# Kernel tuning notes

Hardware: AMD Instinct MI355X
Metric: run time of the kernel (lower is better)

Reference implementation:

```python
import jax, jax.numpy as jnp
import numpy as np

B, T_IN, F_IN, H, T_OUT = 1024, 168, 8, 256, 96


def setup_inputs() -> dict:
    key = jax.random.key(0)
    ks = jax.random.split(key, 12)
    s = 1.0 / np.sqrt(H)  # torch LSTM/Linear default init scale
    return {
        "inputs": jax.random.normal(ks[0], (B, T_IN, F_IN), jnp.float32),
        "enc_Wih": jax.random.normal(ks[1], (4 * H, F_IN), jnp.float32) * s,
        "enc_Whh": jax.random.normal(ks[2], (4 * H, H), jnp.float32) * s,
        "enc_bih": jax.random.normal(ks[3], (4 * H,), jnp.float32) * s,
        "enc_bhh": jax.random.normal(ks[4], (4 * H,), jnp.float32) * s,
        "dec_Wih": jax.random.normal(ks[5], (4 * H, 1), jnp.float32) * s,
        "dec_Whh": jax.random.normal(ks[6], (4 * H, H), jnp.float32) * s,
        "dec_bih": jax.random.normal(ks[7], (4 * H,), jnp.float32) * s,
        "dec_bhh": jax.random.normal(ks[8], (4 * H,), jnp.float32) * s,
        "fc_W": jax.random.normal(ks[9], (1, H), jnp.float32) * s,
        "fc_b": jax.random.normal(ks[10], (1,), jnp.float32) * s,
    }


def _lstm_cell(x, h, c, Wih, Whh, bih, bhh):
    # PyTorch gate order: input, forget, cell(g), output
    gates = x @ Wih.T + h @ Whh.T + (bih + bhh)  # [B, 4H]
    i, f, g, o = jnp.split(gates, 4, axis=-1)
    c_new = jax.nn.sigmoid(f) * c + jax.nn.sigmoid(i) * jnp.tanh(g)
    h_new = jax.nn.sigmoid(o) * jnp.tanh(c_new)
    return h_new, c_new


def reference(inputs, enc_Wih, enc_Whh, enc_bih, enc_bhh,
              dec_Wih, dec_Whh, dec_bih, dec_bhh, fc_W, fc_b):
    batch = inputs.shape[0]
    hidden = inputs.shape[1] and enc_Whh.shape[1]
    h0 = jnp.zeros((batch, enc_Whh.shape[1]), inputs.dtype)
    c0 = jnp.zeros_like(h0)

    # ---- encoder: scan over input time steps ----
    def enc_step(carry, x_t):
        h, c = carry
        h, c = _lstm_cell(x_t, h, c, enc_Wih, enc_Whh, enc_bih, enc_bhh)
        return (h, c), None

    (h, c), _ = jax.lax.scan(enc_step, (h0, c0),
                             jnp.swapaxes(inputs, 0, 1))  # [T,B,F]

    x0 = inputs[:, -1, 0:1]  # [B,1] last value of main feature

    def dec_step(carry, _):
        x, h, c = carry
        h, c = _lstm_cell(x, h, c, dec_Wih, dec_Whh, dec_bih, dec_bhh)
        pred = h @ fc_W.T + fc_b  # [B,1]
        return (pred, h, c), pred

    _, preds = jax.lax.scan(dec_step, (x0, h, c), None, length=T_OUT)
    # preds: [T_OUT, B, 1] -> [B, T_OUT, 1]
    return jnp.swapaxes(preds, 0, 1)
```

## Files before the change

kernel.cpp:

```cpp
#include <hip/hip_runtime.h>


typedef _Float16 f16x8 __attribute__((ext_vector_type(8)));
typedef float f32x4 __attribute__((ext_vector_type(4)));

#define WPW  36864
#define NSTEPS_ENC 168
#define NSTEPS_DEC 96

__device__ __forceinline__ float sigm(float x) {
    float e = __builtin_amdgcn_exp2f(-1.4426950408889634f * x);
    return __builtin_amdgcn_rcpf(1.0f + e);
}
__device__ __forceinline__ float tanh_f(float x) {
    float e = __builtin_amdgcn_exp2f(-2.8853900817779268f * x);
    return 2.0f * __builtin_amdgcn_rcpf(1.0f + e) - 1.0f;
}

__device__ __forceinline__ void mfma8(f32x4 acc[8], f16x8 a, const f16x8 b[8]) {
#pragma unroll
    for (int nt = 0; nt < 8; ++nt)
        acc[nt] = __builtin_amdgcn_mfma_f32_16x16x32_f16(a, b[nt], acc[nt], 0, 0, 0);
}

__device__ __forceinline__ void gemm_all(f32x4 acc[8],
                                         const f16x8 wr[5][8],
                                         const f16x8 (*Bw)[64],
                                         const f16x8 (*K8w)[16],
                                         const _Float16* __restrict__ wp,
                                         const char* ab, int abase,
                                         const _Float16* xsrow,
                                         int lane, int l15, int lg) {
    f16x8 s5[8];
#pragma unroll
    for (int nt = 0; nt < 8; ++nt)
        s5[nt] = *(const f16x8*)(wp + ((5 * 8 + nt) * 64 + lane) * 8);

#pragma unroll
    for (int kt = 0; kt < 5; ++kt) {
        f16x8 a = *(const f16x8*)(ab + abase + kt * 64);
        mfma8(acc, a, wr[kt]);
    }
    {
        f16x8 a = *(const f16x8*)(ab + abase + 5 * 64);
        mfma8(acc, a, s5);
    }
#pragma unroll
    for (int kt = 6; kt < 8; ++kt) {
        f16x8 a = *(const f16x8*)(ab + abase + kt * 64);
#pragma unroll
        for (int nt = 0; nt < 8; ++nt)
            acc[nt] = __builtin_amdgcn_mfma_f32_16x16x32_f16(a, Bw[(kt - 6) * 8 + nt][lane], acc[nt], 0, 0, 0);
    }
    {
        f16x8 a = *(const f16x8*)xsrow;
        _Float16 m = (_Float16)(lg == 0 ? 1.0f : 0.0f);
#pragma unroll
        for (int nt = 0; nt < 8; ++nt) {
            f16x8 b = K8w[nt][l15] * m;
            acc[nt] = __builtin_amdgcn_mfma_f32_16x16x32_f16(a, b, acc[nt], 0, 0, 0);
        }
    }
}


__global__ void k_convert_x(const float* __restrict__ in, _Float16* __restrict__ xf16) {
    int idx = blockIdx.x * 256 + threadIdx.x;
    if (idx >= 168 * 1024 * 8) return;
    int f = idx & 7;
    int b = (idx >> 3) & 1023;
    int t = idx >> 13;
    xf16[idx] = (_Float16)in[(b * 168 + t) * 8 + f];
}

__global__ void k_pack_w(const float* __restrict__ Whh, const float* __restrict__ Wih,
                         int IN, _Float16* __restrict__ Wp) {
    int idx = blockIdx.x * 256 + threadIdx.x;
    if (idx >= 294912) return;
    int j    = idx & 7;
    int lane = (idx >> 3) & 63;
    int nt   = (idx >> 9) & 7;
    int kt   = (idx >> 12) % 9;
    int wv   = idx / 36864;
    int n = (nt >> 1) * 256 + wv * 32 + (nt & 1) * 16 + (lane & 15);
    int k = kt * 32 + (lane >> 4) * 8 + j;
    float v = 0.0f;
    if (k < 256)            v = Whh[n * 256 + k];
    else if (k - 256 < IN)  v = Wih[n * IN + (k - 256)];
    Wp[idx] = (_Float16)v;
}


__global__ __launch_bounds__(512, 2) void lstm_seq2seq(
    const _Float16* __restrict__ xf16,
    const _Float16* __restrict__ WpE,
    const _Float16* __restrict__ WpD,
    const float* __restrict__ bihE, const float* __restrict__ bhhE,
    const float* __restrict__ bihD, const float* __restrict__ bhhD,
    const float* __restrict__ fcW,
    const float* __restrict__ fcb,
    float* __restrict__ out) {

    __shared__ f16x8 Blds[8][16][64];
    __shared__ f16x8 K8[8][8][16];
    __shared__ _Float16 Abuf[16 * 256];
    __shared__ _Float16 xs[16][8];
    __shared__ float partial[8][16];

    const int tid  = threadIdx.x;
    const int lane = tid & 63;
    const int wv   = tid >> 6;
    const int l15  = lane & 15;
    const int lg   = lane >> 4;
    const int b0   = blockIdx.x * 16;

    const char* ab = (const char*)Abuf;
    const int abase = l15 * 512 + ((lg * 16) ^ ((l15 & 3) << 4));

    for (int i = tid; i < 16 * 256; i += 512) Abuf[i] = (_Float16)0.0f;

    const _Float16* wpe = WpE + wv * WPW;
    const _Float16* wpd = WpD + wv * WPW;

    f16x8 wr[5][8];
#pragma unroll
    for (int kt = 0; kt < 5; ++kt)
#pragma unroll
        for (int nt = 0; nt < 8; ++nt)
            wr[kt][nt] = *(const f16x8*)(wpe + ((kt * 8 + nt) * 64 + lane) * 8);
#pragma unroll
    for (int kt = 6; kt < 8; ++kt)
#pragma unroll
        for (int nt = 0; nt < 8; ++nt)
            Blds[wv][(kt - 6) * 8 + nt][lane] = *(const f16x8*)(wpe + ((kt * 8 + nt) * 64 + lane) * 8);
    if (lane < 16) {
#pragma unroll
        for (int nt = 0; nt < 8; ++nt)
            K8[wv][nt][lane] = *(const f16x8*)(wpe + ((8 * 8 + nt) * 64 + lane) * 8);
    }
    float bia[8];
#pragma unroll
    for (int nt = 0; nt < 8; ++nt) {
        int n = (nt >> 1) * 256 + wv * 32 + (nt & 1) * 16 + l15;
        bia[nt] = bihE[n] + bhhE[n];
    }

    float c_st[2][4] = {{0.f,0.f,0.f,0.f},{0.f,0.f,0.f,0.f}};

    __syncthreads();
    if (tid < 128) {
        int m = tid >> 3, f = tid & 7;
        xs[m][f] = xf16[(size_t)(b0 + m) * 8 + f];
    }
    __syncthreads();

#pragma unroll 1
    for (int t = 0; t < NSTEPS_ENC; ++t) {
        f32x4 acc[8];
#pragma unroll
        for (int nt = 0; nt < 8; ++nt) { f32x4 z = {0.f,0.f,0.f,0.f}; acc[nt] = z; }

        _Float16 xh = (_Float16)0.0f;
        if (t < NSTEPS_ENC - 1 && tid < 128)
            xh = xf16[(size_t)((t + 1) * 1024 + b0 + (tid >> 3)) * 8 + (tid & 7)];

        gemm_all(acc, wr, Blds[wv], K8[wv], wpe, ab, abase, &xs[l15][0], lane, l15, lg);

        float hnv[2][4];
#pragma unroll
        for (int half = 0; half < 2; ++half) {
#pragma unroll
            for (int r = 0; r < 4; ++r) {
                float iv = acc[0 + half][r] + bia[0 + half];
                float fv = acc[2 + half][r] + bia[2 + half];
                float gv = acc[4 + half][r] + bia[4 + half];
                float ov = acc[6 + half][r] + bia[6 + half];
                float cn = sigm(fv) * c_st[half][r] + sigm(iv) * tanh_f(gv);
                c_st[half][r] = cn;
                hnv[half][r] = sigm(ov) * tanh_f(cn);
            }
        }
        __syncthreads();
#pragma unroll
        for (int half = 0; half < 2; ++half) {
#pragma unroll
            for (int r = 0; r < 4; ++r) {
                int row = lg * 4 + r;
                int colb = (wv * 32 + half * 16 + l15) * 2;
                *(_Float16*)((char*)Abuf + row * 512 + (colb ^ ((r & 3) << 4))) = (_Float16)hnv[half][r];
            }
        }
        if (t < NSTEPS_ENC - 1) {
            if (tid < 128) xs[tid >> 3][tid & 7] = xh;
        } else {
            if (tid < 16) {
#pragma unroll
                for (int f = 1; f < 8; ++f) xs[tid][f] = (_Float16)0.0f;
            }
        }
        __syncthreads();
    }

#pragma unroll
    for (int kt = 0; kt < 5; ++kt)
#pragma unroll
        for (int nt = 0; nt < 8; ++nt)
            wr[kt][nt] = *(const f16x8*)(wpd + ((kt * 8 + nt) * 64 + lane) * 8);
#pragma unroll
    for (int kt = 6; kt < 8; ++kt)
#pragma unroll
        for (int nt = 0; nt < 8; ++nt)
            Blds[wv][(kt - 6) * 8 + nt][lane] = *(const f16x8*)(wpd + ((kt * 8 + nt) * 64 + lane) * 8);
    if (lane < 16) {
#pragma unroll
        for (int nt = 0; nt < 8; ++nt)
            K8[wv][nt][lane] = *(const f16x8*)(wpd + ((8 * 8 + nt) * 64 + lane) * 8);
    }
#pragma unroll
    for (int nt = 0; nt < 8; ++nt) {
        int n = (nt >> 1) * 256 + wv * 32 + (nt & 1) * 16 + l15;
        bia[nt] = bihD[n] + bhhD[n];
    }
    float fcw0 = fcW[wv * 32 + l15];
    float fcw1 = fcW[wv * 32 + 16 + l15];
    float fcbv = fcb[0];
    __syncthreads();

#pragma unroll 1
    for (int s = 0; s < NSTEPS_DEC; ++s) {
        f32x4 acc[8];
#pragma unroll
        for (int nt = 0; nt < 8; ++nt) { f32x4 z = {0.f,0.f,0.f,0.f}; acc[nt] = z; }

        gemm_all(acc, wr, Blds[wv], K8[wv], wpd, ab, abase, &xs[l15][0], lane, l15, lg);

        float hnv[2][4];
#pragma unroll
        for (int half = 0; half < 2; ++half) {
#pragma unroll
            for (int r = 0; r < 4; ++r) {
                float iv = acc[0 + half][r] + bia[0 + half];
                float fv = acc[2 + half][r] + bia[2 + half];
                float gv = acc[4 + half][r] + bia[4 + half];
                float ov = acc[6 + half][r] + bia[6 + half];
                float cn = sigm(fv) * c_st[half][r] + sigm(iv) * tanh_f(gv);
                c_st[half][r] = cn;
                hnv[half][r] = sigm(ov) * tanh_f(cn);
            }
        }
#pragma unroll
        for (int r = 0; r < 4; ++r) {
            float pv = hnv[0][r] * fcw0 + hnv[1][r] * fcw1;
            pv += __shfl_xor(pv, 1);
            pv += __shfl_xor(pv, 2);
            pv += __shfl_xor(pv, 4);
            pv += __shfl_xor(pv, 8);
            if (l15 == 0) partial[wv][lg * 4 + r] = pv;
        }
        __syncthreads();
#pragma unroll
        for (int half = 0; half < 2; ++half) {
#pragma unroll
            for (int r = 0; r < 4; ++r) {
                int row = lg * 4 + r;
                int colb = (wv * 32 + half * 16 + l15) * 2;
                *(_Float16*)((char*)Abuf + row * 512 + (colb ^ ((r & 3) << 4))) = (_Float16)hnv[half][r];
            }
        }
        if (tid < 16) {
            float pr = fcbv;
#pragma unroll
            for (int w = 0; w < 8; ++w) pr += partial[w][tid];
            out[(size_t)(b0 + tid) * 96 + s] = pr;
            xs[tid][0] = (_Float16)pr;
        }
        __syncthreads();
    }
}


extern "C" void kernel_launch(void* const* d_in, const int* in_sizes, int n_in,
                              void* d_out, int out_size, void* d_ws, size_t ws_size,
                              hipStream_t stream) {
    const float* inputs  = (const float*)d_in[0];
    const float* enc_Wih = (const float*)d_in[1];
    const float* enc_Whh = (const float*)d_in[2];
    const float* enc_bih = (const float*)d_in[3];
    const float* enc_bhh = (const float*)d_in[4];
    const float* dec_Wih = (const float*)d_in[5];
    const float* dec_Whh = (const float*)d_in[6];
    const float* dec_bih = (const float*)d_in[7];
    const float* dec_bhh = (const float*)d_in[8];
    const float* fc_W    = (const float*)d_in[9];
    const float* fc_b    = (const float*)d_in[10];

    char* ws = (char*)d_ws;
    _Float16* xf16 = (_Float16*)(ws);
    _Float16* WpE  = (_Float16*)(ws + 2752512);
    _Float16* WpD  = (_Float16*)(ws + 2752512 + 589824);

    k_convert_x<<<dim3(5376), dim3(256), 0, stream>>>(inputs, xf16);
    k_pack_w<<<dim3(1152), dim3(256), 0, stream>>>(enc_Whh, enc_Wih, 8, WpE);
    k_pack_w<<<dim3(1152), dim3(256), 0, stream>>>(dec_Whh, dec_Wih, 1, WpD);

    lstm_seq2seq<<<dim3(64), dim3(512), 0, stream>>>(
        xf16, WpE, WpD, enc_bih, enc_bhh, dec_bih, dec_bhh, fc_W, fc_b, (float*)d_out);
}
```

Baseline: 1.123 ms.

## Double-buffer hidden state and fuse encoder/decoder loops with one barrier per step

Merges the encoder and decoder loops into one time loop and double-buffers the hidden-state LDS tile, the input tile and the FC partials, so each step needs one __syncthreads instead of two. It folds the bias into the accumulator init and adds the scalar decoder input as an FMA in fp32 rather than an extra MFMA tile. It also redistributes the FC reduction so every wave recomputes the prediction locally, and changes the LDS swizzle to an 8-way XOR. A leftover dead kernel stub with placeholder assignments remains, and the unified loop adds branches on the encoder/decoder flag.

```diff
diff --git a/kernel.cpp b/kernel.cpp
--- a/kernel.cpp
+++ b/kernel.cpp
@@ -5,8 +5,8 @@
 typedef float f32x4 __attribute__((ext_vector_type(4)));
 
 #define WPW  36864
-#define NSTEPS_ENC 168
-#define NSTEPS_DEC 96
+#define NENC 168
+#define NTOT 264
 
 __device__ __forceinline__ float sigm(float x) {
     float e = __builtin_amdgcn_exp2f(-1.4426950408889634f * x);
@@ -16,51 +16,12 @@
     float e = __builtin_amdgcn_exp2f(-2.8853900817779268f * x);
     return 2.0f * __builtin_amdgcn_rcpf(1.0f + e) - 1.0f;
 }
-
+__device__ __forceinline__ f32x4 mfma(f16x8 a, f16x8 b, f32x4 c) {
+    return __builtin_amdgcn_mfma_f32_16x16x32_f16(a, b, c, 0, 0, 0);
+}
 __device__ __forceinline__ void mfma8(f32x4 acc[8], f16x8 a, const f16x8 b[8]) {
 #pragma unroll
-    for (int nt = 0; nt < 8; ++nt)
-        acc[nt] = __builtin_amdgcn_mfma_f32_16x16x32_f16(a, b[nt], acc[nt], 0, 0, 0);
-}
-
-__device__ __forceinline__ void gemm_all(f32x4 acc[8],
-                                         const f16x8 wr[5][8],
-                                         const f16x8 (*Bw)[64],
-                                         const f16x8 (*K8w)[16],
-                                         const _Float16* __restrict__ wp,
-                                         const char* ab, int abase,
-                                         const _Float16* xsrow,
-                                         int lane, int l15, int lg) {
-    f16x8 s5[8];
-#pragma unroll
-    for (int nt = 0; nt < 8; ++nt)
-        s5[nt] = *(const f16x8*)(wp + ((5 * 8 + nt) * 64 + lane) * 8);
-
-#pragma unroll
-    for (int kt = 0; kt < 5; ++kt) {
-        f16x8 a = *(const f16x8*)(ab + abase + kt * 64);
-        mfma8(acc, a, wr[kt]);
-    }
-    {
-        f16x8 a = *(const f16x8*)(ab + abase + 5 * 64);
-        mfma8(acc, a, s5);
-    }
-#pragma unroll
-    for (int kt = 6; kt < 8; ++kt) {
-        f16x8 a = *(const f16x8*)(ab + abase + kt * 64);
-#pragma unroll
-        for (int nt = 0; nt < 8; ++nt)
-            acc[nt] = __builtin_amdgcn_mfma_f32_16x16x32_f16(a, Bw[(kt - 6) * 8 + nt][lane], acc[nt], 0, 0, 0);
-    }
-    {
-        f16x8 a = *(const f16x8*)xsrow;
-        _Float16 m = (_Float16)(lg == 0 ? 1.0f : 0.0f);
-#pragma unroll
-        for (int nt = 0; nt < 8; ++nt) {
-            f16x8 b = K8w[nt][l15] * m;
-            acc[nt] = __builtin_amdgcn_mfma_f32_16x16x32_f16(a, b, acc[nt], 0, 0, 0);
-        }
-    }
+    for (int nt = 0; nt < 8; ++nt) acc[nt] = mfma(a, b[nt], acc[nt]);
 }
 
 
@@ -91,21 +52,20 @@
 }
 
 
-__global__ __launch_bounds__(512, 2) void lstm_seq2seq(
+__global__ __launch_bounds__(512, 2) void lstm6(
+    const float* __restrict__ in0,
     const _Float16* __restrict__ xf16,
     const _Float16* __restrict__ WpE,
     const _Float16* __restrict__ WpD,
     const float* __restrict__ bihE, const float* __restrict__ bhhE,
     const float* __restrict__ bihD, const float* __restrict__ bhhD,
-    const float* __restrict__ fcW,
-    const float* __restrict__ fcb,
+    const float* __restrict__ fcW, const float* __restrict__ fcb,
     float* __restrict__ out) {
 
     __shared__ f16x8 Blds[8][16][64];
-    __shared__ f16x8 K8[8][8][16];
-    __shared__ _Float16 Abuf[16 * 256];
-    __shared__ _Float16 xs[16][8];
-    __shared__ float partial[8][16];
+    __shared__ _Float16 A[2][16 * 256];
+    __shared__ f16x8 xs[2][16];
+    __shared__ f32x4 partial[2][16][2];
 
     const int tid  = threadIdx.x;
     const int lane = tid & 63;
@@ -114,169 +74,214 @@
     const int lg   = lane >> 4;
     const int b0   = blockIdx.x * 16;
 
-    const char* ab = (const char*)Abuf;
-    const int abase = l15 * 512 + ((lg * 16) ^ ((l15 & 3) << 4));
-
-    for (int i = tid; i < 16 * 256; i += 512) Abuf[i] = (_Float16)0.0f;
-
     const _Float16* wpe = WpE + wv * WPW;
     const _Float16* wpd = WpD + wv * WPW;
+    const _Float16* wp8 = wpe + 64 * 512;
 
     f16x8 wr[5][8];
 #pragma unroll
     for (int kt = 0; kt < 5; ++kt)
 #pragma unroll
         for (int nt = 0; nt < 8; ++nt)
-            wr[kt][nt] = *(const f16x8*)(wpe + ((kt * 8 + nt) * 64 + lane) * 8);
+            wr[kt][nt] = *(const f16x8*)(wpe + (size_t)(kt * 8 + nt) * 512 + lane * 8);
 #pragma unroll
     for (int kt = 6; kt < 8; ++kt)
 #pragma unroll
         for (int nt = 0; nt < 8; ++nt)
-            Blds[wv][(kt - 6) * 8 + nt][lane] = *(const f16x8*)(wpe + ((kt * 8 + nt) * 64 + lane) * 8);
-    if (lane < 16) {
-#pragma unroll
-        for (int nt = 0; nt < 8; ++nt)
-            K8[wv][nt][lane] = *(const f16x8*)(wpe + ((8 * 8 + nt) * 64 + lane) * 8);
-    }
+            Blds[wv][(kt - 6) * 8 + nt][lane] = *(const f16x8*)(wpe + (size_t)(kt * 8 + nt) * 512 + lane * 8);
+
     float bia[8];
 #pragma unroll
     for (int nt = 0; nt < 8; ++nt) {
         int n = (nt >> 1) * 256 + wv * 32 + (nt & 1) * 16 + l15;
         bia[nt] = bihE[n] + bhhE[n];
     }
+    const float fcw0 = fcW[wv * 32 + l15];
+    const float fcw1 = fcW[wv * 32 + 16 + l15];
+    const float fcbv = fcb[0];
+
+    int aaddr[8];
+#pragma unroll
+    for (int kt = 0; kt < 8; ++kt)
+        aaddr[kt] = l15 * 512 + ((((kt * 4 + lg) ^ (l15 & 7)) & 31) << 4);
+
+    for (int i = tid; i < 16 * 256; i += 512) A[0][i] = (_Float16)0.0f;
+    if (tid < 128)
+        ((_Float16*)&xs[0][tid >> 3])[tid & 7] = xf16[(size_t)(b0 + (tid >> 3)) * 8 + (tid & 7)];
 
     float c_st[2][4] = {{0.f,0.f,0.f,0.f},{0.f,0.f,0.f,0.f}};
+    float wih_s[8] = {0,0,0,0,0,0,0,0};
+    float pred[4]  = {0,0,0,0};
 
     __syncthreads();
-    if (tid < 128) {
-        int m = tid >> 3, f = tid & 7;
-        xs[m][f] = xf16[(size_t)(b0 + m) * 8 + f];
-    }
-    __syncthreads();
 
 #pragma unroll 1
-    for (int t = 0; t < NSTEPS_ENC; ++t) {
+    for (int it = 0; it < NTOT; ++it) {
+        const bool enc = (it < NENC);
+        const int rb = it & 1, wbuf = rb ^ 1;
+        const char* ab = (const char*)&A[0][0] + rb * 8192;
+        char*       aw = (char*)&A[0][0] + wbuf * 8192;
+        const _Float16* wp = enc ? wpe : wpd;
+
+        if (it == NENC) {
+#pragma unroll
+            for (int kt = 0; kt < 5; ++kt)
+#pragma unroll
+                for (int nt = 0; nt < 8; ++nt)
+                    wr[kt][nt] = *(const f16x8*)(wpd + (size_t)(kt * 8 + nt) * 512 + lane * 8);
+#pragma unroll
+            for (int kt = 6; kt < 8; ++kt)
+#pragma unroll
+                for (int nt = 0; nt < 8; ++nt)
+                    Blds[wv][(kt - 6) * 8 + nt][lane] = *(const f16x8*)(wpd + (size_t)(kt * 8 + nt) * 512 + lane * 8);
+#pragma unroll
+            for (int nt = 0; nt < 8; ++nt) {
+                int n = (nt >> 1) * 256 + wv * 32 + (nt & 1) * 16 + l15;
+                bia[nt]   = bihD[n] + bhhD[n];
+                wih_s[nt] = ((const float*)bihD == nullptr) ? 0.f : 0.f;
+            }
+#pragma unroll
+            for (int nt = 0; nt < 8; ++nt) {
+                int n = (nt >> 1) * 256 + wv * 32 + (nt & 1) * 16 + l15;
+                wih_s[nt] = fcb == nullptr ? 0.f : 0.f;
+            }
+#pragma unroll
+            for (int nt = 0; nt < 8; ++nt) {
+                int n = (nt >> 1) * 256 + wv * 32 + (nt & 1) * 16 + l15;
+                wih_s[nt] = __ldg(&bhhD[0]) * 0.f;
+            }
+            ;
+#pragma unroll
+            for (int r = 0; r < 4; ++r)
+                pred[r] = in0[((size_t)(b0 + lg * 4 + r) * 168 + 167) * 8 + 0];
+        }
+
         f32x4 acc[8];
-#pragma unroll
-        for (int nt = 0; nt < 8; ++nt) { f32x4 z = {0.f,0.f,0.f,0.f}; acc[nt] = z; }
-
-        _Float16 xh = (_Float16)0.0f;
-        if (t < NSTEPS_ENC - 1 && tid < 128)
-            xh = xf16[(size_t)((t + 1) * 1024 + b0 + (tid >> 3)) * 8 + (tid & 7)];
-
-        gemm_all(acc, wr, Blds[wv], K8[wv], wpe, ab, abase, &xs[l15][0], lane, l15, lg);
+        if (enc) {
+#pragma unroll
+            for (int nt = 0; nt < 8; ++nt) { f32x4 v = {bia[nt], bia[nt], bia[nt], bia[nt]}; acc[nt] = v; }
+        } else {
+            if (it > NENC) {
+#pragma unroll
+                for (int r = 0; r < 4; ++r) {
+                    const int row = lg * 4 + r;
+                    f32x4 pa = partial[rb][row][0];
+                    f32x4 pb = partial[rb][row][1];
+                    pred[r] = fcbv + (((pa[0] + pa[1]) + (pa[2] + pa[3]))
+                                    + ((pb[0] + pb[1]) + (pb[2] + pb[3])));
+                    if (wv == 0 && l15 == 0)
+                        out[(size_t)(b0 + row) * 96 + (it - NENC - 1)] = pred[r];
+                }
+            }
+#pragma unroll
+            for (int nt = 0; nt < 8; ++nt) {
+                f32x4 v;
+#pragma unroll
+                for (int r = 0; r < 4; ++r) v[r] = __builtin_fmaf(wih_s[nt], pred[r], bia[nt]);
+                acc[nt] = v;
+            }
+        }
+
+        f16x8 s5[8];
+#pragma unroll
+        for (int nt = 0; nt < 8; ++nt)
+            s5[nt] = *(const f16x8*)(wp + (size_t)(5 * 8 + nt) * 512 + lane * 8);
+
+        _Float16 xreg = (_Float16)0.0f;
+        if (enc && it < NENC - 1 && tid < 128)
+            xreg = xf16[(size_t)((it + 1) * 1024 + b0 + (tid >> 3)) * 8 + (tid & 7)];
+
+#pragma unroll
+        for (int kt = 0; kt < 5; ++kt) {
+            f16x8 a = *(const f16x8*)(ab + aaddr[kt]);
+            mfma8(acc, a, wr[kt]);
+        }
+        {
+            f16x8 a = *(const f16x8*)(ab + aaddr[5]);
+            mfma8(acc, a, s5);
+        }
+        __builtin_amdgcn_sched_barrier(0);
+        f16x8 k8b[8];
+        if (enc) {
+#pragma unroll
+            for (int nt = 0; nt < 8; ++nt)
+                k8b[nt] = *(const f16x8*)(wp8 + (size_t)nt * 512 + l15 * 8);
+        }
+#pragma unroll
+        for (int kt = 6; kt < 8; ++kt) {
+            f16x8 a = *(const f16x8*)(ab + aaddr[kt]);
+#pragma unroll
+            for (int nt = 0; nt < 8; ++nt)
+                acc[nt] = mfma(a, Blds[wv][(kt - 6) * 8 + nt][lane], acc[nt]);
+        }
+        if (enc) {
+            f16x8 a8 = xs[rb][l15];
+            _Float16 m = (_Float16)(lg == 0 ? 1.0f : 0.0f);
+            a8 = a8 * m;
+            mfma8(acc, a8, k8b);
+        }
 
         float hnv[2][4];
 #pragma unroll
         for (int half = 0; half < 2; ++half) {
 #pragma unroll
             for (int r = 0; r < 4; ++r) {
-                float iv = acc[0 + half][r] + bia[0 + half];
-                float fv = acc[2 + half][r] + bia[2 + half];
-                float gv = acc[4 + half][r] + bia[4 + half];
-                float ov = acc[6 + half][r] + bia[6 + half];
+                float iv = acc[0 + half][r];
+                float fv = acc[2 + half][r];
+                float gv = acc[4 + half][r];
+                float ov = acc[6 + half][r];
                 float cn = sigm(fv) * c_st[half][r] + sigm(iv) * tanh_f(gv);
                 c_st[half][r] = cn;
-                hnv[half][r] = sigm(ov) * tanh_f(cn);
-            }
-        }
-        __syncthreads();
-#pragma unroll
-        for (int half = 0; half < 2; ++half) {
+                float hn = sigm(ov) * tanh_f(cn);
+                hnv[half][r] = hn;
+                int row  = lg * 4 + r;
+                int colb = (wv * 32 + half * 16 + l15) * 2;
+                *(_Float16*)(aw + row * 512 + (colb ^ ((row & 7) << 4))) = (_Float16)hn;
+            }
+        }
+
+        if (!enc) {
 #pragma unroll
             for (int r = 0; r < 4; ++r) {
-                int row = lg * 4 + r;
-                int colb = (wv * 32 + half * 16 + l15) * 2;
-                *(_Float16*)((char*)Abuf + row * 512 + (colb ^ ((r & 3) << 4))) = (_Float16)hnv[half][r];
-            }
-        }
-        if (t < NSTEPS_ENC - 1) {
-            if (tid < 128) xs[tid >> 3][tid & 7] = xh;
-        } else {
-            if (tid < 16) {
-#pragma unroll
-                for (int f = 1; f < 8; ++f) xs[tid][f] = (_Float16)0.0f;
-            }
-        }
+                float pv = hnv[0][r] * fcw0 + hnv[1][r] * fcw1;
+                pv += __shfl_xor(pv, 1);
+                pv += __shfl_xor(pv, 2);
+                pv += __shfl_xor(pv, 4);
+                pv += __shfl_xor(pv, 8);
+                if (l15 == 0)
+                    ((float*)&partial[wbuf][lg * 4 + r][0])[wv] = pv;
+            }
+        } else if (it < NENC - 1) {
+            if (tid < 128)
+                ((_Float16*)&xs[wbuf][tid >> 3])[tid & 7] = xreg;
+        }
+
         __syncthreads();
     }
 
-#pragma unroll
-    for (int kt = 0; kt < 5; ++kt)
-#pragma unroll
-        for (int nt = 0; nt < 8; ++nt)
-            wr[kt][nt] = *(const f16x8*)(wpd + ((kt * 8 + nt) * 64 + lane) * 8);
-#pragma unroll
-    for (int kt = 6; kt < 8; ++kt)
-#pragma unroll
-        for (int nt = 0; nt < 8; ++nt)
-            Blds[wv][(kt - 6) * 8 + nt][lane] = *(const f16x8*)(wpd + ((kt * 8 + nt) * 64 + lane) * 8);
-    if (lane < 16) {
-#pragma unroll
-        for (int nt = 0; nt < 8; ++nt)
-            K8[wv][nt][lane] = *(const f16x8*)(wpd + ((8 * 8 + nt) * 64 + lane) * 8);
+    if (wv == 0 && l15 == 0) {
+#pragma unroll
+        for (int r = 0; r < 4; ++r) {
+            const int row = lg * 4 + r;
+            f32x4 pa = partial[0][row][0];
+            f32x4 pb = partial[0][row][1];
+            float pr = fcbv + (((pa[0] + pa[1]) + (pa[2] + pa[3]))
+                             + ((pb[0] + pb[1]) + (pb[2] + pb[3])));
+            out[(size_t)(b0 + row) * 96 + 95] = pr;
+        }
     }
-#pragma unroll
-    for (int nt = 0; nt < 8; ++nt) {
-        int n = (nt >> 1) * 256 + wv * 32 + (nt & 1) * 16 + l15;
-        bia[nt] = bihD[n] + bhhD[n];
-    }
-    float fcw0 = fcW[wv * 32 + l15];
-    float fcw1 = fcW[wv * 32 + 16 + l15];
-    float fcbv = fcb[0];
-    __syncthreads();
-
-#pragma unroll 1
-    for (int s = 0; s < NSTEPS_DEC; ++s) {
-        f32x4 acc[8];
-#pragma unroll
-        for (int nt = 0; nt < 8; ++nt) { f32x4 z = {0.f,0.f,0.f,0.f}; acc[nt] = z; }
-
-        gemm_all(acc, wr, Blds[wv], K8[wv], wpd, ab, abase, &xs[l15][0], lane, l15, lg);
-
-        float hnv[2][4];
-#pragma unroll
-        for (int half = 0; half < 2; ++half) {
-#pragma unroll
-            for (int r = 0; r < 4; ++r) {
-                float iv = acc[0 + half][r] + bia[0 + half];
-                float fv = acc[2 + half][r] + bia[2 + half];
-                float gv = acc[4 + half][r] + bia[4 + half];
-                float ov = acc[6 + half][r] + bia[6 + half];
-                float cn = sigm(fv) * c_st[half][r] + sigm(iv) * tanh_f(gv);
-                c_st[half][r] = cn;
-                hnv[half][r] = sigm(ov) * tanh_f(cn);
-            }
-        }
-#pragma unroll
-        for (int r = 0; r < 4; ++r) {
-            float pv = hnv[0][r] * fcw0 + hnv[1][r] * fcw1;
-            pv += __shfl_xor(pv, 1);
-            pv += __shfl_xor(pv, 2);
-            pv += __shfl_xor(pv, 4);
-            pv += __shfl_xor(pv, 8);
-            if (l15 == 0) partial[wv][lg * 4 + r] = pv;
-        }
-        __syncthreads();
-#pragma unroll
-        for (int half = 0; half < 2; ++half) {
-#pragma unroll
-            for (int r = 0; r < 4; ++r) {
-                int row = lg * 4 + r;
-                int colb = (wv * 32 + half * 16 + l15) * 2;
-                *(_Float16*)((char*)Abuf + row * 512 + (colb ^ ((r & 3) << 4))) = (_Float16)hnv[half][r];
-            }
-        }
-        if (tid < 16) {
-            float pr = fcbv;
-#pragma unroll
-            for (int w = 0; w < 8; ++w) pr += partial[w][tid];
-            out[(size_t)(b0 + tid) * 96 + s] = pr;
-            xs[tid][0] = (_Float16)pr;
-        }
-        __syncthreads();
-    }
-}
+}
+
+__global__ __launch_bounds__(512, 2) void lstm6_full(
+    const float* __restrict__ in0,
+    const _Float16* __restrict__ xf16,
+    const _Float16* __restrict__ WpE,
+    const _Float16* __restrict__ WpD,
+    const float* __restrict__ bihE, const float* __restrict__ bhhE,
+    const float* __restrict__ bihD, const float* __restrict__ bhhD,
+    const float* __restrict__ dWih,
+    const float* __restrict__ fcW, const float* __restrict__ fcb,
+    float* __restrict__ out);
 
 
 extern "C" void kernel_launch(void* const* d_in, const int* in_sizes, int n_in,
@@ -303,6 +308,218 @@
     k_pack_w<<<dim3(1152), dim3(256), 0, stream>>>(enc_Whh, enc_Wih, 8, WpE);
     k_pack_w<<<dim3(1152), dim3(256), 0, stream>>>(dec_Whh, dec_Wih, 1, WpD);
 
-    lstm_seq2seq<<<dim3(64), dim3(512), 0, stream>>>(
-        xf16, WpE, WpD, enc_bih, enc_bhh, dec_bih, dec_bhh, fc_W, fc_b, (float*)d_out);
-}
+    lstm6_full<<<dim3(64), dim3(512), 0, stream>>>(
+        inputs, xf16, WpE, WpD, enc_bih, enc_bhh, dec_bih, dec_bhh,
+        dec_Wih, fc_W, fc_b, (float*)d_out);
+}
+
+
+__global__ __launch_bounds__(512, 2) void lstm6_full(
+    const float* __restrict__ in0,
+    const _Float16* __restrict__ xf16,
+    const _Float16* __restrict__ WpE,
+    const _Float16* __restrict__ WpD,
+    const float* __restrict__ bihE, const float* __restrict__ bhhE,
+    const float* __restrict__ bihD, const float* __restrict__ bhhD,
+    const float* __restrict__ dWih,
+    const float* __restrict__ fcW, const float* __restrict__ fcb,
+    float* __restrict__ out) {
+
+    __shared__ f16x8 Blds[8][16][64];
+    __shared__ _Float16 A[2][16 * 256];
+    __shared__ f16x8 xs[2][16];
+    __shared__ f32x4 partial[2][16][2];
+
+    const int tid  = threadIdx.x;
+    const int lane = tid & 63;
+    const int wv   = tid >> 6;
+    const int l15  = lane & 15;
+    const int lg   = lane >> 4;
+    const int b0   = blockIdx.x * 16;
+
+    const _Float16* wpe = WpE + wv * WPW;
+    const _Float16* wpd = WpD + wv * WPW;
+    const _Float16* wp8 = wpe + 64 * 512;
+
+    f16x8 wr[5][8];
+#pragma unroll
+    for (int kt = 0; kt < 5; ++kt)
+#pragma unroll
+        for (int nt = 0; nt < 8; ++nt)
+            wr[kt][nt] = *(const f16x8*)(wpe + (size_t)(kt * 8 + nt) * 512 + lane * 8);
+#pragma unroll
+    for (int kt = 6; kt < 8; ++kt)
+#pragma unroll
+        for (int nt = 0; nt < 8; ++nt)
+            Blds[wv][(kt - 6) * 8 + nt][lane] = *(const f16x8*)(wpe + (size_t)(kt * 8 + nt) * 512 + lane * 8);
+
+    float bia[8];
+#pragma unroll
+    for (int nt = 0; nt < 8; ++nt) {
+        int n = (nt >> 1) * 256 + wv * 32 + (nt & 1) * 16 + l15;
+        bia[nt] = bihE[n] + bhhE[n];
+    }
+    const float fcw0 = fcW[wv * 32 + l15];
+    const float fcw1 = fcW[wv * 32 + 16 + l15];
+    const float fcbv = fcb[0];
+
+    int aaddr[8];
+#pragma unroll
+    for (int kt = 0; kt < 8; ++kt)
+        aaddr[kt] = l15 * 512 + ((((kt * 4 + lg) ^ (l15 & 7)) & 31) << 4);
+
+    for (int i = tid; i < 16 * 256; i += 512) A[0][i] = (_Float16)0.0f;
+    if (tid < 128)
+        ((_Float16*)&xs[0][tid >> 3])[tid & 7] = xf16[(size_t)(b0 + (tid >> 3)) * 8 + (tid & 7)];
+
+    float c_st[2][4] = {{0.f,0.f,0.f,0.f},{0.f,0.f,0.f,0.f}};
+    float wih_s[8] = {0,0,0,0,0,0,0,0};
+    float pred[4]  = {0,0,0,0};
+
+    __syncthreads();
+
+#pragma unroll 1
+    for (int it = 0; it < NTOT; ++it) {
+        const bool enc = (it < NENC);
+        const int rb = it & 1, wbuf = rb ^ 1;
+        const char* ab = (const char*)&A[0][0] + rb * 8192;
+        char*       aw = (char*)&A[0][0] + wbuf * 8192;
+        const _Float16* wp = enc ? wpe : wpd;
+
+        if (it == NENC) {
+#pragma unroll
+            for (int kt = 0; kt < 5; ++kt)
+#pragma unroll
+                for (int nt = 0; nt < 8; ++nt)
+                    wr[kt][nt] = *(const f16x8*)(wpd + (size_t)(kt * 8 + nt) * 512 + lane * 8);
+#pragma unroll
+            for (int kt = 6; kt < 8; ++kt)
+#pragma unroll
+                for (int nt = 0; nt < 8; ++nt)
+                    Blds[wv][(kt - 6) * 8 + nt][lane] = *(const f16x8*)(wpd + (size_t)(kt * 8 + nt) * 512 + lane * 8);
+#pragma unroll
+            for (int nt = 0; nt < 8; ++nt) {
+                int n = (nt >> 1) * 256 + wv * 32 + (nt & 1) * 16 + l15;
+                bia[nt]   = bihD[n] + bhhD[n];
+                wih_s[nt] = dWih[n];
+            }
+#pragma unroll
+            for (int r = 0; r < 4; ++r)
+                pred[r] = in0[((size_t)(b0 + lg * 4 + r) * 168 + 167) * 8 + 0];
+        }
+
+        f32x4 acc[8];
+        if (enc) {
+#pragma unroll
+            for (int nt = 0; nt < 8; ++nt) { f32x4 v = {bia[nt], bia[nt], bia[nt], bia[nt]}; acc[nt] = v; }
+        } else {
+            if (it > NENC) {
+#pragma unroll
+                for (int r = 0; r < 4; ++r) {
+                    const int row = lg * 4 + r;
+                    f32x4 pa = partial[rb][row][0];
+                    f32x4 pb = partial[rb][row][1];
+                    pred[r] = fcbv + (((pa[0] + pa[1]) + (pa[2] + pa[3]))
+                                    + ((pb[0] + pb[1]) + (pb[2] + pb[3])));
+                    if (wv == 0 && l15 == 0)
+                        out[(size_t)(b0 + row) * 96 + (it - NENC - 1)] = pred[r];
+                }
+            }
+#pragma unroll
+            for (int nt = 0; nt < 8; ++nt) {
+                f32x4 v;
+#pragma unroll
+                for (int r = 0; r < 4; ++r) v[r] = __builtin_fmaf(wih_s[nt], pred[r], bia[nt]);
+                acc[nt] = v;
+            }
+        }
+
+        f16x8 s5[8];
+#pragma unroll
+        for (int nt = 0; nt < 8; ++nt)
+            s5[nt] = *(const f16x8*)(wp + (size_t)(5 * 8 + nt) * 512 + lane * 8);
+
+        _Float16 xreg = (_Float16)0.0f;
+        if (enc && it < NENC - 1 && tid < 128)
+            xreg = xf16[(size_t)((it + 1) * 1024 + b0 + (tid >> 3)) * 8 + (tid & 7)];
+
+#pragma unroll
+        for (int kt = 0; kt < 5; ++kt) {
+            f16x8 a = *(const f16x8*)(ab + aaddr[kt]);
+            mfma8(acc, a, wr[kt]);
+        }
+        {
+            f16x8 a = *(const f16x8*)(ab + aaddr[5]);
+            mfma8(acc, a, s5);
+        }
+        __builtin_amdgcn_sched_barrier(0);
+        f16x8 k8b[8];
+        if (enc) {
+#pragma unroll
+            for (int nt = 0; nt < 8; ++nt)
+                k8b[nt] = *(const f16x8*)(wp8 + (size_t)nt * 512 + l15 * 8);
+        }
+#pragma unroll
+        for (int kt = 6; kt < 8; ++kt) {
+            f16x8 a = *(const f16x8*)(ab + aaddr[kt]);
+#pragma unroll
+            for (int nt = 0; nt < 8; ++nt)
+                acc[nt] = mfma(a, Blds[wv][(kt - 6) * 8 + nt][lane], acc[nt]);
+        }
+        if (enc) {
+            f16x8 a8 = xs[rb][l15];
+            _Float16 m = (_Float16)(lg == 0 ? 1.0f : 0.0f);
+            a8 = a8 * m;
+            mfma8(acc, a8, k8b);
+        }
+
+        float hnv[2][4];
+#pragma unroll
+        for (int half = 0; half < 2; ++half) {
+#pragma unroll
+            for (int r = 0; r < 4; ++r) {
+                float iv = acc[0 + half][r];
+                float fv = acc[2 + half][r];
+                float gv = acc[4 + half][r];
+                float ov = acc[6 + half][r];
+                float cn = sigm(fv) * c_st[half][r] + sigm(iv) * tanh_f(gv);
+                c_st[half][r] = cn;
+                float hn = sigm(ov) * tanh_f(cn);
+                hnv[half][r] = hn;
+                int row  = lg * 4 + r;
+                int colb = (wv * 32 + half * 16 + l15) * 2;
+                *(_Float16*)(aw + row * 512 + (colb ^ ((row & 7) << 4))) = (_Float16)hn;
+            }
+        }
+
+        if (!enc) {
+#pragma unroll
+            for (int r = 0; r < 4; ++r) {
+                float pv = hnv[0][r] * fcw0 + hnv[1][r] * fcw1;
+                pv += __shfl_xor(pv, 1);
+                pv += __shfl_xor(pv, 2);
+                pv += __shfl_xor(pv, 4);
+                pv += __shfl_xor(pv, 8);
+                if (l15 == 0)
+                    ((float*)&partial[wbuf][lg * 4 + r][0])[wv] = pv;
+            }
+        } else if (it < NENC - 1) {
+            if (tid < 128)
+                ((_Float16*)&xs[wbuf][tid >> 3])[tid & 7] = xreg;
+        }
+
+        __syncthreads();
+    }
+
+    if (wv == 0 && l15 == 0) {
+#pragma unroll
+        for (int r = 0; r < 4; ++r) {
+            const int row = lg * 4 + r;
+            f32x4 pa = partial[0][row][0];
+            f32x4 pb = partial[0][row][1];
+            float pr = fcbv + (((pa[0] + pa[1]) + (pa[2] + pa[3]))
+                             + ((pb[0] + pb[1]) + (pb[2] + pb[3])));
+            out[(size_t)(b0 + row) * 96 + 95] = pr;
+        }
+    }
+}
```

Result: slower. 2.450 ms (+118.2%).

## Double-buffer hidden state to use one barrier per step, fold bias and decoder input

Applied to the files above, without the earlier changes.

Keeps the hidden-state tile and the input/partial buffers in two LDS copies so each timestep writes the next buffer directly and needs only one __syncthreads instead of two. Bias is folded into the accumulator initialisation. In the decoder, the scalar input term becomes an FMA with fp32 dec_Wih and the previous prediction, which each wave rebuilds from double-buffered partial sums, replacing the masked K8 MFMA. Encoder input weights now stay in registers, and the LDS swizzle uses a wider XOR pattern. The extra registers and LDS may affect occupancy, and the decoder feedback now stays in fp32 rather than fp16.

```diff
diff --git a/kernel.cpp b/kernel.cpp
--- a/kernel.cpp
+++ b/kernel.cpp
@@ -5,8 +5,8 @@
 typedef float f32x4 __attribute__((ext_vector_type(4)));
 
 #define WPW  36864
-#define NSTEPS_ENC 168
-#define NSTEPS_DEC 96
+#define NENC 168
+#define NDEC 96
 
 __device__ __forceinline__ float sigm(float x) {
     float e = __builtin_amdgcn_exp2f(-1.4426950408889634f * x);
@@ -16,51 +16,12 @@
     float e = __builtin_amdgcn_exp2f(-2.8853900817779268f * x);
     return 2.0f * __builtin_amdgcn_rcpf(1.0f + e) - 1.0f;
 }
-
+__device__ __forceinline__ f32x4 mfma(f16x8 a, f16x8 b, f32x4 c) {
+    return __builtin_amdgcn_mfma_f32_16x16x32_f16(a, b, c, 0, 0, 0);
+}
 __device__ __forceinline__ void mfma8(f32x4 acc[8], f16x8 a, const f16x8 b[8]) {
 #pragma unroll
-    for (int nt = 0; nt < 8; ++nt)
-        acc[nt] = __builtin_amdgcn_mfma_f32_16x16x32_f16(a, b[nt], acc[nt], 0, 0, 0);
-}
-
-__device__ __forceinline__ void gemm_all(f32x4 acc[8],
-                                         const f16x8 wr[5][8],
-                                         const f16x8 (*Bw)[64],
-                                         const f16x8 (*K8w)[16],
-                                         const _Float16* __restrict__ wp,
-                                         const char* ab, int abase,
-                                         const _Float16* xsrow,
-                                         int lane, int l15, int lg) {
-    f16x8 s5[8];
-#pragma unroll
-    for (int nt = 0; nt < 8; ++nt)
-        s5[nt] = *(const f16x8*)(wp + ((5 * 8 + nt) * 64 + lane) * 8);
-
-#pragma unroll
-    for (int kt = 0; kt < 5; ++kt) {
-        f16x8 a = *(const f16x8*)(ab + abase + kt * 64);
-        mfma8(acc, a, wr[kt]);
-    }
-    {
-        f16x8 a = *(const f16x8*)(ab + abase + 5 * 64);
-        mfma8(acc, a, s5);
-    }
-#pragma unroll
-    for (int kt = 6; kt < 8; ++kt) {
-        f16x8 a = *(const f16x8*)(ab + abase + kt * 64);
-#pragma unroll
-        for (int nt = 0; nt < 8; ++nt)
-            acc[nt] = __builtin_amdgcn_mfma_f32_16x16x32_f16(a, Bw[(kt - 6) * 8 + nt][lane], acc[nt], 0, 0, 0);
-    }
-    {
-        f16x8 a = *(const f16x8*)xsrow;
-        _Float16 m = (_Float16)(lg == 0 ? 1.0f : 0.0f);
-#pragma unroll
-        for (int nt = 0; nt < 8; ++nt) {
-            f16x8 b = K8w[nt][l15] * m;
-            acc[nt] = __builtin_amdgcn_mfma_f32_16x16x32_f16(a, b, acc[nt], 0, 0, 0);
-        }
-    }
+    for (int nt = 0; nt < 8; ++nt) acc[nt] = mfma(a, b[nt], acc[nt]);
 }
 
 
@@ -91,21 +52,21 @@
 }
 
 
-__global__ __launch_bounds__(512, 2) void lstm_seq2seq(
+__global__ __launch_bounds__(512, 2) void lstm7(
+    const float* __restrict__ in0,
     const _Float16* __restrict__ xf16,
     const _Float16* __restrict__ WpE,
     const _Float16* __restrict__ WpD,
     const float* __restrict__ bihE, const float* __restrict__ bhhE,
     const float* __restrict__ bihD, const float* __restrict__ bhhD,
-    const float* __restrict__ fcW,
-    const float* __restrict__ fcb,
+    const float* __restrict__ dWih,
+    const float* __restrict__ fcW, const float* __restrict__ fcb,
     float* __restrict__ out) {
 
     __shared__ f16x8 Blds[8][16][64];
-    __shared__ f16x8 K8[8][8][16];
-    __shared__ _Float16 Abuf[16 * 256];
-    __shared__ _Float16 xs[16][8];
-    __shared__ float partial[8][16];
+    __shared__ _Float16 A[2][16 * 256];
+    __shared__ f16x8 xs[2][16];
+    __shared__ f32x4 partial[2][16][2];
 
     const int tid  = threadIdx.x;
     const int lane = tid & 63;
@@ -114,138 +75,199 @@
     const int lg   = lane >> 4;
     const int b0   = blockIdx.x * 16;
 
-    const char* ab = (const char*)Abuf;
-    const int abase = l15 * 512 + ((lg * 16) ^ ((l15 & 3) << 4));
-
-    for (int i = tid; i < 16 * 256; i += 512) Abuf[i] = (_Float16)0.0f;
-
     const _Float16* wpe = WpE + wv * WPW;
     const _Float16* wpd = WpD + wv * WPW;
 
-    f16x8 wr[5][8];
+    f16x8 wr[6][8];
 #pragma unroll
     for (int kt = 0; kt < 5; ++kt)
 #pragma unroll
         for (int nt = 0; nt < 8; ++nt)
-            wr[kt][nt] = *(const f16x8*)(wpe + ((kt * 8 + nt) * 64 + lane) * 8);
+            wr[kt][nt] = *(const f16x8*)(wpe + (size_t)(kt * 8 + nt) * 512 + lane * 8);
+#pragma unroll
+    for (int nt = 0; nt < 8; ++nt)
+        wr[5][nt] = *(const f16x8*)(wpe + (size_t)(8 * 8 + nt) * 512 + lane * 8);
 #pragma unroll
     for (int kt = 6; kt < 8; ++kt)
 #pragma unroll
         for (int nt = 0; nt < 8; ++nt)
-            Blds[wv][(kt - 6) * 8 + nt][lane] = *(const f16x8*)(wpe + ((kt * 8 + nt) * 64 + lane) * 8);
-    if (lane < 16) {
-#pragma unroll
-        for (int nt = 0; nt < 8; ++nt)
-            K8[wv][nt][lane] = *(const f16x8*)(wpe + ((8 * 8 + nt) * 64 + lane) * 8);
-    }
+            Blds[wv][(kt - 6) * 8 + nt][lane] = *(const f16x8*)(wpe + (size_t)(kt * 8 + nt) * 512 + lane * 8);
+
     float bia[8];
 #pragma unroll
     for (int nt = 0; nt < 8; ++nt) {
         int n = (nt >> 1) * 256 + wv * 32 + (nt & 1) * 16 + l15;
         bia[nt] = bihE[n] + bhhE[n];
     }
+    const float fcw0 = fcW[wv * 32 + l15];
+    const float fcw1 = fcW[wv * 32 + 16 + l15];
+    const float fcbv = fcb[0];
+
+    int aaddr[8];
+#pragma unroll
+    for (int kt = 0; kt < 8; ++kt)
+        aaddr[kt] = l15 * 512 + ((((kt * 4 + lg) ^ (l15 & 7)) & 31) << 4);
+
+    for (int i = tid; i < 16 * 256; i += 512) A[0][i] = (_Float16)0.0f;
+    if (tid < 128)
+        ((_Float16*)&xs[0][tid >> 3])[tid & 7] = xf16[(size_t)(b0 + (tid >> 3)) * 8 + (tid & 7)];
 
     float c_st[2][4] = {{0.f,0.f,0.f,0.f},{0.f,0.f,0.f,0.f}};
 
     __syncthreads();
-    if (tid < 128) {
-        int m = tid >> 3, f = tid & 7;
-        xs[m][f] = xf16[(size_t)(b0 + m) * 8 + f];
-    }
-    __syncthreads();
 
 #pragma unroll 1
-    for (int t = 0; t < NSTEPS_ENC; ++t) {
+    for (int it = 0; it < NENC; ++it) {
+        const int rb = it & 1, wbuf = rb ^ 1;
+        const char* ab = (const char*)&A[0][0] + rb * 8192;
+        char*       aw = (char*)&A[0][0] + wbuf * 8192;
+
         f32x4 acc[8];
 #pragma unroll
-        for (int nt = 0; nt < 8; ++nt) { f32x4 z = {0.f,0.f,0.f,0.f}; acc[nt] = z; }
-
-        _Float16 xh = (_Float16)0.0f;
-        if (t < NSTEPS_ENC - 1 && tid < 128)
-            xh = xf16[(size_t)((t + 1) * 1024 + b0 + (tid >> 3)) * 8 + (tid & 7)];
-
-        gemm_all(acc, wr, Blds[wv], K8[wv], wpe, ab, abase, &xs[l15][0], lane, l15, lg);
-
-        float hnv[2][4];
+        for (int nt = 0; nt < 8; ++nt) { f32x4 v = {bia[nt], bia[nt], bia[nt], bia[nt]}; acc[nt] = v; }
+
+        f16x8 s5[8];
+#pragma unroll
+        for (int nt = 0; nt < 8; ++nt)
+            s5[nt] = *(const f16x8*)(wpe + (size_t)(5 * 8 + nt) * 512 + lane * 8);
+
+        _Float16 xreg = (_Float16)0.0f;
+        if (it < NENC - 1 && tid < 128)
+            xreg = xf16[(size_t)((it + 1) * 1024 + b0 + (tid >> 3)) * 8 + (tid & 7)];
+
+#pragma unroll
+        for (int kt = 0; kt < 5; ++kt) {
+            f16x8 a = *(const f16x8*)(ab + aaddr[kt]);
+            mfma8(acc, a, wr[kt]);
+        }
+        {
+            f16x8 a = *(const f16x8*)(ab + aaddr[5]);
+            mfma8(acc, a, s5);
+        }
+#pragma unroll
+        for (int kt = 6; kt < 8; ++kt) {
+            f16x8 a = *(const f16x8*)(ab + aaddr[kt]);
+#pragma unroll
+            for (int nt = 0; nt < 8; ++nt)
+                acc[nt] = mfma(a, Blds[wv][(kt - 6) * 8 + nt][lane], acc[nt]);
+        }
+        {
+            f16x8 a = xs[rb][l15];
+            mfma8(acc, a, wr[5]);
+        }
+
 #pragma unroll
         for (int half = 0; half < 2; ++half) {
 #pragma unroll
             for (int r = 0; r < 4; ++r) {
-                float iv = acc[0 + half][r] + bia[0 + half];
-                float fv = acc[2 + half][r] + bia[2 + half];
-                float gv = acc[4 + half][r] + bia[4 + half];
-                float ov = acc[6 + half][r] + bia[6 + half];
+                float iv = acc[0 + half][r];
+                float fv = acc[2 + half][r];
+                float gv = acc[4 + half][r];
+                float ov = acc[6 + half][r];
                 float cn = sigm(fv) * c_st[half][r] + sigm(iv) * tanh_f(gv);
                 c_st[half][r] = cn;
-                hnv[half][r] = sigm(ov) * tanh_f(cn);
+                float hn = sigm(ov) * tanh_f(cn);
+                int row  = lg * 4 + r;
+                int colb = (wv * 32 + half * 16 + l15) * 2;
+                *(_Float16*)(aw + row * 512 + (colb ^ ((row & 7) << 4))) = (_Float16)hn;
             }
         }
+        if (it < NENC - 1 && tid < 128)
+            ((_Float16*)&xs[wbuf][tid >> 3])[tid & 7] = xreg;
+
         __syncthreads();
-#pragma unroll
-        for (int half = 0; half < 2; ++half) {
-#pragma unroll
-            for (int r = 0; r < 4; ++r) {
-                int row = lg * 4 + r;
-                int colb = (wv * 32 + half * 16 + l15) * 2;
-                *(_Float16*)((char*)Abuf + row * 512 + (colb ^ ((r & 3) << 4))) = (_Float16)hnv[half][r];
-            }
-        }
-        if (t < NSTEPS_ENC - 1) {
-            if (tid < 128) xs[tid >> 3][tid & 7] = xh;
-        } else {
-            if (tid < 16) {
-#pragma unroll
-                for (int f = 1; f < 8; ++f) xs[tid][f] = (_Float16)0.0f;
-            }
-        }
-        __syncthreads();
     }
 
 #pragma unroll
     for (int kt = 0; kt < 5; ++kt)
 #pragma unroll
         for (int nt = 0; nt < 8; ++nt)
-            wr[kt][nt] = *(const f16x8*)(wpd + ((kt * 8 + nt) * 64 + lane) * 8);
+            wr[kt][nt] = *(const f16x8*)(wpd + (size_t)(kt * 8 + nt) * 512 + lane * 8);
 #pragma unroll
     for (int kt = 6; kt < 8; ++kt)
 #pragma unroll
         for (int nt = 0; nt < 8; ++nt)
-            Blds[wv][(kt - 6) * 8 + nt][lane] = *(const f16x8*)(wpd + ((kt * 8 + nt) * 64 + lane) * 8);
-    if (lane < 16) {
-#pragma unroll
-        for (int nt = 0; nt < 8; ++nt)
-            K8[wv][nt][lane] = *(const f16x8*)(wpd + ((8 * 8 + nt) * 64 + lane) * 8);
-    }
+            Blds[wv][(kt - 6) * 8 + nt][lane] = *(const f16x8*)(wpd + (size_t)(kt * 8 + nt) * 512 + lane * 8);
+
+    float wih_s[8];
 #pragma unroll
     for (int nt = 0; nt < 8; ++nt) {
         int n = (nt >> 1) * 256 + wv * 32 + (nt & 1) * 16 + l15;
-        bia[nt] = bihD[n] + bhhD[n];
-    }
-    float fcw0 = fcW[wv * 32 + l15];
-    float fcw1 = fcW[wv * 32 + 16 + l15];
-    float fcbv = fcb[0];
-    __syncthreads();
+        bia[nt]   = bihD[n] + bhhD[n];
+        wih_s[nt] = dWih[n];
+    }
+    float pred[4];
+#pragma unroll
+    for (int r = 0; r < 4; ++r)
+        pred[r] = in0[((size_t)(b0 + lg * 4 + r) * 168 + 167) * 8 + 0];
 
 #pragma unroll 1
-    for (int s = 0; s < NSTEPS_DEC; ++s) {
+    for (int s = 0; s < NDEC; ++s) {
+        const int it = NENC + s;
+        const int rb = it & 1, wbuf = rb ^ 1;
+        const char* ab = (const char*)&A[0][0] + rb * 8192;
+        char*       aw = (char*)&A[0][0] + wbuf * 8192;
+
+        if (s > 0) {
+#pragma unroll
+            for (int r = 0; r < 4; ++r) {
+                const int row = lg * 4 + r;
+                f32x4 pa = partial[rb][row][0];
+                f32x4 pb = partial[rb][row][1];
+                pred[r] = fcbv + (((pa[0] + pa[1]) + (pa[2] + pa[3]))
+                                + ((pb[0] + pb[1]) + (pb[2] + pb[3])));
+                if (wv == 0 && l15 == 0)
+                    out[(size_t)(b0 + row) * 96 + (s - 1)] = pred[r];
+            }
+        }
+
         f32x4 acc[8];
 #pragma unroll
-        for (int nt = 0; nt < 8; ++nt) { f32x4 z = {0.f,0.f,0.f,0.f}; acc[nt] = z; }
-
-        gemm_all(acc, wr, Blds[wv], K8[wv], wpd, ab, abase, &xs[l15][0], lane, l15, lg);
+        for (int nt = 0; nt < 8; ++nt) {
+            f32x4 v;
+#pragma unroll
+            for (int r = 0; r < 4; ++r) v[r] = __builtin_fmaf(wih_s[nt], pred[r], bia[nt]);
+            acc[nt] = v;
+        }
+
+        f16x8 s5[8];
+#pragma unroll
+        for (int nt = 0; nt < 8; ++nt)
+            s5[nt] = *(const f16x8*)(wpd + (size_t)(5 * 8 + nt) * 512 + lane * 8);
+
+#pragma unroll
+        for (int kt = 0; kt < 5; ++kt) {
+            f16x8 a = *(const f16x8*)(ab + aaddr[kt]);
+            mfma8(acc, a, wr[kt]);
+        }
+        {
+            f16x8 a = *(const f16x8*)(ab + aaddr[5]);
+            mfma8(acc, a, s5);
+        }
+#pragma unroll
+        for (int kt = 6; kt < 8; ++kt) {
+            f16x8 a = *(const f16x8*)(ab + aaddr[kt]);
+#pragma unroll
+            for (int nt = 0; nt < 8; ++nt)
+                acc[nt] = mfma(a, Blds[wv][(kt - 6) * 8 + nt][lane], acc[nt]);
+        }
 
         float hnv[2][4];
 #pragma unroll
         for (int half = 0; half < 2; ++half) {
 #pragma unroll
             for (int r = 0; r < 4; ++r) {
-                float iv = acc[0 + half][r] + bia[0 + half];
-                float fv = acc[2 + half][r] + bia[2 + half];
-                float gv = acc[4 + half][r] + bia[4 + half];
-                float ov = acc[6 + half][r] + bia[6 + half];
+                float iv = acc[0 + half][r];
+                float fv = acc[2 + half][r];
+                float gv = acc[4 + half][r];
+                float ov = acc[6 + half][r];
                 float cn = sigm(fv) * c_st[half][r] + sigm(iv) * tanh_f(gv);
                 c_st[half][r] = cn;
-                hnv[half][r] = sigm(ov) * tanh_f(cn);
+                float hn = sigm(ov) * tanh_f(cn);
+                hnv[half][r] = hn;
+                int row  = lg * 4 + r;
+                int colb = (wv * 32 + half * 16 + l15) * 2;
+                *(_Float16*)(aw + row * 512 + (colb ^ ((row & 7) << 4))) = (_Float16)hn;
             }
         }
 #pragma unroll
@@ -255,26 +277,23 @@
             pv += __shfl_xor(pv, 2);
             pv += __shfl_xor(pv, 4);
             pv += __shfl_xor(pv, 8);
-            if (l15 == 0) partial[wv][lg * 4 + r] = pv;
-        }
+            if (l15 == 0)
+                ((float*)&partial[wbuf][lg * 4 + r][0])[wv] = pv;
+        }
+
         __syncthreads();
-#pragma unroll
-        for (int half = 0; half < 2; ++half) {
-#pragma unroll
-            for (int r = 0; r < 4; ++r) {
-                int row = lg * 4 + r;
-                int colb = (wv * 32 + half * 16 + l15) * 2;
-                *(_Float16*)((char*)Abuf + row * 512 + (colb ^ ((r & 3) << 4))) = (_Float16)hnv[half][r];
-            }
-        }
-        if (tid < 16) {
-            float pr = fcbv;
-#pragma unroll
-            for (int w = 0; w < 8; ++w) pr += partial[w][tid];
-            out[(size_t)(b0 + tid) * 96 + s] = pr;
-            xs[tid][0] = (_Float16)pr;
-        }
-        __syncthreads();
+    }
+
+    if (wv == 0 && l15 == 0) {
+#pragma unroll
+        for (int r = 0; r < 4; ++r) {
+            const int row = lg * 4 + r;
+            f32x4 pa = partial[0][row][0];
+            f32x4 pb = partial[0][row][1];
+            float pr = fcbv + (((pa[0] + pa[1]) + (pa[2] + pa[3]))
+                             + ((pb[0] + pb[1]) + (pb[2] + pb[3])));
+            out[(size_t)(b0 + row) * 96 + 95] = pr;
+        }
     }
 }
 
@@ -303,6 +322,7 @@
     k_pack_w<<<dim3(1152), dim3(256), 0, stream>>>(enc_Whh, enc_Wih, 8, WpE);
     k_pack_w<<<dim3(1152), dim3(256), 0, stream>>>(dec_Whh, dec_Wih, 1, WpD);
 
-    lstm_seq2seq<<<dim3(64), dim3(512), 0, stream>>>(
-        xf16, WpE, WpD, enc_bih, enc_bhh, dec_bih, dec_bhh, fc_W, fc_b, (float*)d_out);
-}
+    lstm7<<<dim3(64), dim3(512), 0, stream>>>(
+        inputs, xf16, WpE, WpD, enc_bih, enc_bhh, dec_bih, dec_bhh,
+        dec_Wih, fc_W, fc_b, (float*)d_out);
+}
```

Result: slower. 1.814 ms (+61.5%).
